# Kernel tuning notes

Measured on AMD Instinct MI355X. Metric: run time of the kernel, lower is better.

## Reference

```python
import jax, jax.numpy as jnp
import numpy as np

B, C, A, H, W = 8, 64, 32, 64, 64  # batch, input_nf, atten_nf, height, width

def setup_inputs() -> dict:
    key = jax.random.key(0)
    k = jax.random.split(key, 5)
    scale = 1.0 / np.sqrt(C)
    return {
        "x":  jax.random.normal(k[0], (B, C, H, W), dtype=jnp.float32),
        "Wg": jax.random.uniform(k[1], (A, C), jnp.float32, -scale, scale),  # 1x1 conv kernel
        "bg": jax.random.uniform(k[2], (A,),   jnp.float32, -scale, scale),
        "Wh": jax.random.uniform(k[3], (A, C), jnp.float32, -scale, scale),
        "bh": jax.random.uniform(k[4], (A,),   jnp.float32, -scale, scale),
    }

def reference(x, Wg, bg, Wh, bh):
    b, c, h, w = x.shape
    n = h * w
    xf = x.reshape(b, c, n)                               # [B, C, N]
    g = jnp.einsum('ac,bcn->ban', Wg, xf) + bg[None, :, None]  # 1x1 conv == GEMM
    hq = jnp.einsum('ac,bcn->ban', Wh, xf) + bh[None, :, None]
    scores = jnp.einsum('ban,bam->bnm', g, hq)            # [B, N, N]
    alpha = jax.nn.softmax(scores, axis=2)
    r = jnp.einsum('bnm,bcm->bcn', alpha, xf)             # alpha @ x^T, back to [B,C,N]
    r = r.reshape(b, c, h, w)
    r = r + x  # is_residual=True
    return (jax.nn.relu(r), alpha)
```

## Files before the change

kernel.cpp:

```cpp
#include <hip/hip_runtime.h>
#include <hip/hip_bf16.h>
#include <math.h>

#define NB 8
#define NC 64
#define NA 32
#define NN 4096
#define NWAVE 8

typedef __attribute__((ext_vector_type(8))) short bf16x8;
typedef __attribute__((ext_vector_type(4))) short bf16x4;
typedef __attribute__((ext_vector_type(4))) float f32x4;

#if __has_builtin(__builtin_amdgcn_mfma_f32_16x16x16bf16_1k)
  #define HAVE_MFMA16 1
  #define MFMA16(A,B,C) __builtin_amdgcn_mfma_f32_16x16x16bf16_1k(A,B,C,0,0,0)
#elif __has_builtin(__builtin_amdgcn_mfma_f32_16x16x16_bf16)
  #define HAVE_MFMA16 1
  #define MFMA16(A,B,C) __builtin_amdgcn_mfma_f32_16x16x16_bf16(A,B,C,0,0,0)
#else
  #define HAVE_MFMA16 0
#endif

__device__ inline ushort f2bf(float f) {
  union { float f; unsigned u; } v; v.f = f;
  unsigned r = v.u + 0x7fffu + ((v.u >> 16) & 1u);
  return (ushort)(r >> 16);
}

__device__ inline bf16x8 pack8(const f32x4 a, const f32x4 b) {
  union { ushort us[8]; bf16x8 v; } u;
#pragma unroll
  for (int i = 0; i < 4; ++i) { u.us[i] = f2bf(a[i]); u.us[4 + i] = f2bf(b[i]); }
  return u.v;
}

__device__ inline uint2 packbf(const f32x4 p) {
  uint2 q;
  q.x = (uint)f2bf(p[0]) | ((uint)f2bf(p[1]) << 16);
  q.y = (uint)f2bf(p[2]) | ((uint)f2bf(p[3]) << 16);
  return q;
}

#if HAVE_MFMA16
__device__ inline bf16x4 pk4(const f32x4 p) {
  union { uint u[2]; bf16x4 v; } t;
  asm("v_cvt_pk_bf16_f32 %0, %1, %2" : "=v"(t.u[0]) : "v"(p[0]), "v"(p[1]));
  asm("v_cvt_pk_bf16_f32 %0, %1, %2" : "=v"(t.u[1]) : "v"(p[2]), "v"(p[3]));
  return t.v;
}
#endif

__global__ __launch_bounds__(256) void prep_kernel(
    const float* __restrict__ x, const float* __restrict__ Wg, const float* __restrict__ bg,
    const float* __restrict__ Wh, const float* __restrict__ bh,
    ushort* __restrict__ gT, ushort* __restrict__ hqT, ushort* __restrict__ xfb2)
{
  __shared__ float wg_s[NA * NC];
  __shared__ float wh_s[NA * NC];
  const int t = threadIdx.x;
  for (int i = t; i < NA * NC; i += 256) { wg_s[i] = Wg[i]; wh_s[i] = Wh[i]; }
  __syncthreads();

  const int gid = blockIdx.x * 256 + t;
  const int b = gid >> 12;
  const int n = gid & (NN - 1);
  const float* xb = x + (size_t)b * NC * NN + n;
  const size_t x2base = (size_t)b * NC * NN + (size_t)(n >> 4) * (NC * 16) + (n & 15);

  float accg[NA], acch[NA];
#pragma unroll
  for (int a = 0; a < NA; ++a) { accg[a] = 0.f; acch[a] = 0.f; }

  for (int c4 = 0; c4 < NC / 4; ++c4) {
    const float xv0 = xb[(size_t)(c4 * 4 + 0) * NN];
    const float xv1 = xb[(size_t)(c4 * 4 + 1) * NN];
    const float xv2 = xb[(size_t)(c4 * 4 + 2) * NN];
    const float xv3 = xb[(size_t)(c4 * 4 + 3) * NN];
    xfb2[x2base + (size_t)(c4 * 4 + 0) * 16] = f2bf(xv0);
    xfb2[x2base + (size_t)(c4 * 4 + 1) * 16] = f2bf(xv1);
    xfb2[x2base + (size_t)(c4 * 4 + 2) * 16] = f2bf(xv2);
    xfb2[x2base + (size_t)(c4 * 4 + 3) * 16] = f2bf(xv3);
#pragma unroll
    for (int a = 0; a < NA; ++a) {
      const float4 wg4 = *(const float4*)&wg_s[a * NC + c4 * 4];
      const float4 wh4 = *(const float4*)&wh_s[a * NC + c4 * 4];
      accg[a] += wg4.x * xv0 + wg4.y * xv1 + wg4.z * xv2 + wg4.w * xv3;
      acch[a] += wh4.x * xv0 + wh4.y * xv1 + wh4.z * xv2 + wh4.w * xv3;
    }
  }

  const float LOG2E = 1.44269504088896340736f;
  ushort og[NA], oh[NA];
#pragma unroll
  for (int a = 0; a < NA; ++a) {
    og[a] = f2bf((accg[a] + bg[a]) * LOG2E);
    oh[a] = f2bf(acch[a] + bh[a]);
  }
  const size_t o = ((size_t)b * NN + n) * NA;
#pragma unroll
  for (int k = 0; k < 4; ++k) {
    uint4 vg, vh;
    vg.x = (uint)og[k*8+0] | ((uint)og[k*8+1] << 16);
    vg.y = (uint)og[k*8+2] | ((uint)og[k*8+3] << 16);
    vg.z = (uint)og[k*8+4] | ((uint)og[k*8+5] << 16);
    vg.w = (uint)og[k*8+6] | ((uint)og[k*8+7] << 16);
    vh.x = (uint)oh[k*8+0] | ((uint)oh[k*8+1] << 16);
    vh.y = (uint)oh[k*8+2] | ((uint)oh[k*8+3] << 16);
    vh.z = (uint)oh[k*8+4] | ((uint)oh[k*8+5] << 16);
    vh.w = (uint)oh[k*8+6] | ((uint)oh[k*8+7] << 16);
    *(uint4*)(gT  + o + k * 8) = vg;
    *(uint4*)(hqT + o + k * 8) = vh;
  }
}

__global__ __launch_bounds__(512, 4) void attn_kernel(
    const ushort* __restrict__ gT, const ushort* __restrict__ hqT,
    const ushort* __restrict__ xfb2, const float* __restrict__ x,
    float* __restrict__ outp, float* __restrict__ alpha)
{
  __shared__ float plds[NWAVE][32][32];
  __shared__ float rtile[32][65];
  __shared__ float Lp[NWAVE][32];
  __shared__ float LinvS[32];
#if !HAVE_MFMA16
  ushort (*pbuf)[32][36] = reinterpret_cast<ushort (*)[32][36]>(&plds[0][0][0]);
#endif

  const int tid = threadIdx.x;
  const int l  = tid & 63;
  const int w  = tid >> 6;
  const int lm = l & 15;
  const int lh = l >> 4;

  const int wgid = (blockIdx.x & 7) * 128 + (blockIdx.x >> 3);
  const int b  = wgid >> 7;
  const int n0 = (wgid & 127) << 5;

  const ushort* gB  = gT   + (size_t)b * NN * NA;
  const ushort* hB  = hqT  + (size_t)b * NN * NA;
  const ushort* xB2 = xfb2 + (size_t)b * NC * NN;

  bf16x8 gb0 = *(const bf16x8*)(gB + (size_t)(n0 + lm) * NA + lh * 8);
  bf16x8 gb1 = *(const bf16x8*)(gB + (size_t)(n0 + 16 + lm) * NA + lh * 8);
  const int mbase = w << 9;
  bf16x8 ha0 = *(const bf16x8*)(hB + (size_t)(mbase + lm) * NA + lh * 8);
  bf16x8 ha1 = *(const bf16x8*)(hB + (size_t)(mbase + 16 + lm) * NA + lh * 8);

  float* rflat = &rtile[0][0];
  for (int i = tid; i < 32 * 65; i += 512) rflat[i] = 0.f;

  const f32x4 zz = {0.f, 0.f, 0.f, 0.f};
  f32x4 racc[2][4];
#pragma unroll
  for (int gi = 0; gi < 2; ++gi)
#pragma unroll
    for (int ci = 0; ci < 4; ++ci) racc[gi][ci] = zz;

  float sume0 = 0.f, sume1 = 0.f;
  for (int mc = 0; mc < 16; ++mc) {
    const int m0 = mbase + (mc << 5);
    const int m1 = mbase + (((mc + 1) & 15) << 5);
    const int t0 = m0 >> 4;
    const bf16x8 na0 = *(const bf16x8*)(hB + (size_t)(m1 + lm) * NA + lh * 8);
    const bf16x8 na1 = *(const bf16x8*)(hB + (size_t)(m1 + 16 + lm) * NA + lh * 8);
#if HAVE_MFMA16
    bf16x4 xv0[4], xv1[4];
#pragma unroll
    for (int ci = 0; ci < 4; ++ci) {
      xv0[ci] = *(const bf16x4*)(xB2 + (size_t)t0       * (NC * 16) + (ci * 16 + lm) * 16 + lh * 4);
      xv1[ci] = *(const bf16x4*)(xB2 + (size_t)(t0 + 1) * (NC * 16) + (ci * 16 + lm) * 16 + lh * 4);
    }
#else
    bf16x8 xv[4];
#pragma unroll
    for (int ci = 0; ci < 4; ++ci)
      xv[ci] = *(const bf16x8*)(xB2 + (size_t)(t0 + (lh >> 1)) * (NC * 16) + (ci * 16 + lm) * 16 + (lh & 1) * 8);
#endif

    const f32x4 s00 = __builtin_amdgcn_mfma_f32_16x16x32_bf16(ha0, gb0, zz, 0, 0, 0);
    const f32x4 s10 = __builtin_amdgcn_mfma_f32_16x16x32_bf16(ha1, gb0, zz, 0, 0, 0);
    const f32x4 s01 = __builtin_amdgcn_mfma_f32_16x16x32_bf16(ha0, gb1, zz, 0, 0, 0);
    const f32x4 s11 = __builtin_amdgcn_mfma_f32_16x16x32_bf16(ha1, gb1, zz, 0, 0, 0);

    f32x4 e00, e10, e01, e11;
#pragma unroll
    for (int r = 0; r < 4; ++r) {
      e00[r] = exp2f(s00[r]);
      e10[r] = exp2f(s10[r]);
      e01[r] = exp2f(s01[r]);
      e11[r] = exp2f(s11[r]);
      sume0 += e00[r] + e10[r];
      sume1 += e01[r] + e11[r];
    }

#if HAVE_MFMA16
    const bf16x4 A00 = pk4(e00);
    const bf16x4 A01 = pk4(e10);
    const bf16x4 A10 = pk4(e01);
    const bf16x4 A11 = pk4(e11);
#pragma unroll
    for (int ci = 0; ci < 4; ++ci) {
      racc[0][ci] = MFMA16(A00, xv0[ci], racc[0][ci]);
      racc[0][ci] = MFMA16(A01, xv1[ci], racc[0][ci]);
      racc[1][ci] = MFMA16(A10, xv0[ci], racc[1][ci]);
      racc[1][ci] = MFMA16(A11, xv1[ci], racc[1][ci]);
    }
#else
    *(uint2*)&pbuf[w][lm][lh * 4]           = packbf(e00);
    *(uint2*)&pbuf[w][lm][16 + lh * 4]      = packbf(e10);
    *(uint2*)&pbuf[w][16 + lm][lh * 4]      = packbf(e01);
    *(uint2*)&pbuf[w][16 + lm][16 + lh * 4] = packbf(e11);
    union UB { uint4 u; bf16x8 v; } ua, ub;
    {
      const uint2 a0 = *(const uint2*)&pbuf[w][lm][lh * 8];
      const uint2 a1 = *(const uint2*)&pbuf[w][lm][lh * 8 + 4];
      ua.u = make_uint4(a0.x, a0.y, a1.x, a1.y);
      const uint2 b0 = *(const uint2*)&pbuf[w][16 + lm][lh * 8];
      const uint2 b1 = *(const uint2*)&pbuf[w][16 + lm][lh * 8 + 4];
      ub.u = make_uint4(b0.x, b0.y, b1.x, b1.y);
    }
#pragma unroll
    for (int ci = 0; ci < 4; ++ci) {
      racc[0][ci] = __builtin_amdgcn_mfma_f32_16x16x32_bf16(ua.v, xv[ci], racc[0][ci], 0, 0, 0);
      racc[1][ci] = __builtin_amdgcn_mfma_f32_16x16x32_bf16(ub.v, xv[ci], racc[1][ci], 0, 0, 0);
    }
#endif
    ha0 = na0; ha1 = na1;
  }

  sume0 += __shfl_xor(sume0, 16); sume0 += __shfl_xor(sume0, 32);
  sume1 += __shfl_xor(sume1, 16); sume1 += __shfl_xor(sume1, 32);
  if (l < 16) { Lp[w][l] = sume0; Lp[w][16 + l] = sume1; }
  __syncthreads();

  float Ls0 = 0.f, Ls1 = 0.f;
#pragma unroll
  for (int ww = 0; ww < NWAVE; ++ww) { Ls0 += Lp[ww][lm]; Ls1 += Lp[ww][16 + lm]; }
  const float blog0 = -log2f(Ls0);
  const float blog1 = -log2f(Ls1);

  if (tid < 32) {
    float s = 0.f;
#pragma unroll
    for (int ww = 0; ww < NWAVE; ++ww) s += Lp[ww][tid];
    LinvS[tid] = 1.0f / s;
  }

#pragma unroll
  for (int gi = 0; gi < 2; ++gi)
#pragma unroll
    for (int ci = 0; ci < 4; ++ci)
#pragma unroll
      for (int r = 0; r < 4; ++r)
        atomicAdd(&rtile[gi * 16 + lh * 4 + r][ci * 16 + lm], racc[gi][ci][r]);
  __syncthreads();

  {
    const int c  = tid >> 3;
    const int j4 = (tid & 7) << 2;
    f32x4 v;
#pragma unroll
    for (int k = 0; k < 4; ++k) v[k] = rtile[j4 + k][c] * LinvS[j4 + k];
    const size_t oo = ((size_t)b * NC + c) * NN + n0 + j4;
    const f32x4 xr = *(const f32x4*)(x + oo);
#pragma unroll
    for (int k = 0; k < 4; ++k) {
      const float t = v[k] + xr[k];
      v[k] = t > 0.f ? t : 0.f;
    }
    __builtin_nontemporal_store(v, (f32x4*)(outp + oo));
  }

  const f32x4 bias0 = {blog0, blog0, blog0, blog0};
  const f32x4 bias1 = {blog1, blog1, blog1, blog1};
  float* aB = alpha + ((size_t)b * NN + n0) * NN;
  const int k7   = lm & 7;
  const int nrow = l >> 3;
  const int uu   = l & 7;

  for (int mc = 0; mc < 16; ++mc) {
    const int m0 = mbase + (mc << 5);
    const int m1 = mbase + (((mc + 1) & 15) << 5);
    const bf16x8 na0 = *(const bf16x8*)(hB + (size_t)(m1 + lm) * NA + lh * 8);
    const bf16x8 na1 = *(const bf16x8*)(hB + (size_t)(m1 + 16 + lm) * NA + lh * 8);

    const f32x4 s00 = __builtin_amdgcn_mfma_f32_16x16x32_bf16(ha0, gb0, bias0, 0, 0, 0);
    const f32x4 s10 = __builtin_amdgcn_mfma_f32_16x16x32_bf16(ha1, gb0, bias0, 0, 0, 0);
    const f32x4 s01 = __builtin_amdgcn_mfma_f32_16x16x32_bf16(ha0, gb1, bias1, 0, 0, 0);
    const f32x4 s11 = __builtin_amdgcn_mfma_f32_16x16x32_bf16(ha1, gb1, bias1, 0, 0, 0);

    f32x4 p00, p10, p01, p11;
#pragma unroll
    for (int r = 0; r < 4; ++r) {
      p00[r] = exp2f(s00[r]);
      p10[r] = exp2f(s10[r]);
      p01[r] = exp2f(s01[r]);
      p11[r] = exp2f(s11[r]);
    }

    *(f32x4*)&plds[w][lm]     [((lh    ) ^ k7) << 2] = p00;
    *(f32x4*)&plds[w][lm]     [((lh + 4) ^ k7) << 2] = p10;
    *(f32x4*)&plds[w][16 + lm][((lh    ) ^ k7) << 2] = p01;
    *(f32x4*)&plds[w][16 + lm][((lh + 4) ^ k7) << 2] = p11;

#pragma unroll
    for (int j = 0; j < 4; ++j) {
      const int row = j * 8 + nrow;
      const f32x4 pv = *(const f32x4*)&plds[w][row][(uu ^ (row & 7)) << 2];
      __builtin_nontemporal_store(pv, (f32x4*)(aB + (size_t)row * NN + m0 + uu * 4));
    }
    ha0 = na0; ha1 = na1;
  }
}

extern "C" void kernel_launch(void* const* d_in, const int* in_sizes, int n_in,
                              void* d_out, int out_size, void* d_ws, size_t ws_size,
                              hipStream_t stream) {
  const float* x  = (const float*)d_in[0];
  const float* Wg = (const float*)d_in[1];
  const float* bg = (const float*)d_in[2];
  const float* Wh = (const float*)d_in[3];
  const float* bh = (const float*)d_in[4];

  float* outp  = (float*)d_out;
  float* alpha = outp + (size_t)NB * NC * NN;

  ushort* gT   = (ushort*)d_ws;
  ushort* hqT  = gT + (size_t)NB * NN * NA;
  ushort* xfb2 = hqT + (size_t)NB * NN * NA;

  prep_kernel<<<NB * NN / 256, 256, 0, stream>>>(x, Wg, bg, Wh, bh, gT, hqT, xfb2);
  attn_kernel<<<NB * (NN / 32), 512, 0, stream>>>(gT, hqT, xfb2, x, outp, alpha);
}
```

Before: 218.9 us.

## Split attention into row-sum/output kernel and separate alpha-writing kernel

Result: slower. 274.2 us (+25.2%).

```diff
diff --git a/kernel.cpp b/kernel.cpp
--- a/kernel.cpp
+++ b/kernel.cpp
@@ -114,17 +114,16 @@
   }
 }
 
-__global__ __launch_bounds__(512, 4) void attn_kernel(
+__global__ __launch_bounds__(512, 4) void rsum_kernel(
     const ushort* __restrict__ gT, const ushort* __restrict__ hqT,
     const ushort* __restrict__ xfb2, const float* __restrict__ x,
     float* __restrict__ outp, float* __restrict__ alpha)
 {
-  __shared__ float plds[NWAVE][32][32];
   __shared__ float rtile[32][65];
   __shared__ float Lp[NWAVE][32];
   __shared__ float LinvS[32];
 #if !HAVE_MFMA16
-  ushort (*pbuf)[32][36] = reinterpret_cast<ushort (*)[32][36]>(&plds[0][0][0]);
+  __shared__ ushort pbuf[NWAVE][32][36];
 #endif
 
   const int tid = threadIdx.x;
@@ -234,17 +233,12 @@
   if (l < 16) { Lp[w][l] = sume0; Lp[w][16 + l] = sume1; }
   __syncthreads();
 
-  float Ls0 = 0.f, Ls1 = 0.f;
-#pragma unroll
-  for (int ww = 0; ww < NWAVE; ++ww) { Ls0 += Lp[ww][lm]; Ls1 += Lp[ww][16 + lm]; }
-  const float blog0 = -log2f(Ls0);
-  const float blog1 = -log2f(Ls1);
-
   if (tid < 32) {
     float s = 0.f;
 #pragma unroll
     for (int ww = 0; ww < NWAVE; ++ww) s += Lp[ww][tid];
     LinvS[tid] = 1.0f / s;
+    alpha[((size_t)b * NN + n0 + tid) * NN] = -log2f(s);
   }
 
 #pragma unroll
@@ -256,25 +250,54 @@
         atomicAdd(&rtile[gi * 16 + lh * 4 + r][ci * 16 + lm], racc[gi][ci][r]);
   __syncthreads();
 
-  {
-    const int c  = tid >> 3;
-    const int j4 = (tid & 7) << 2;
-    f32x4 v;
-#pragma unroll
-    for (int k = 0; k < 4; ++k) v[k] = rtile[j4 + k][c] * LinvS[j4 + k];
-    const size_t oo = ((size_t)b * NC + c) * NN + n0 + j4;
-    const f32x4 xr = *(const f32x4*)(x + oo);
-#pragma unroll
-    for (int k = 0; k < 4; ++k) {
-      const float t = v[k] + xr[k];
-      v[k] = t > 0.f ? t : 0.f;
-    }
-    __builtin_nontemporal_store(v, (f32x4*)(outp + oo));
-  }
-
-  const f32x4 bias0 = {blog0, blog0, blog0, blog0};
-  const f32x4 bias1 = {blog1, blog1, blog1, blog1};
+  const int c  = tid >> 3;
+  const int j4 = (tid & 7) << 2;
+  f32x4 v;
+#pragma unroll
+  for (int k = 0; k < 4; ++k) v[k] = rtile[j4 + k][c] * LinvS[j4 + k];
+  const size_t oo = ((size_t)b * NC + c) * NN + n0 + j4;
+  const f32x4 xr = *(const f32x4*)(x + oo);
+#pragma unroll
+  for (int k = 0; k < 4; ++k) {
+    const float t = v[k] + xr[k];
+    v[k] = t > 0.f ? t : 0.f;
+  }
+  __builtin_nontemporal_store(v, (f32x4*)(outp + oo));
+}
+
+__global__ __launch_bounds__(512) void alpha_kernel(
+    const ushort* __restrict__ gT, const ushort* __restrict__ hqT,
+    float* __restrict__ alpha)
+{
+  __shared__ float plds[NWAVE][32][32];
+
+  const int tid = threadIdx.x;
+  const int l  = tid & 63;
+  const int w  = tid >> 6;
+  const int lm = l & 15;
+  const int lh = l >> 4;
+
+  const int wgid = (blockIdx.x & 7) * 128 + (blockIdx.x >> 3);
+  const int b  = wgid >> 7;
+  const int n0 = (wgid & 127) << 5;
+
+  const ushort* gB = gT  + (size_t)b * NN * NA;
+  const ushort* hB = hqT + (size_t)b * NN * NA;
   float* aB = alpha + ((size_t)b * NN + n0) * NN;
+
+  const float bl0 = aB[(size_t)lm * NN];
+  const float bl1 = aB[(size_t)(16 + lm) * NN];
+
+  bf16x8 gb0 = *(const bf16x8*)(gB + (size_t)(n0 + lm) * NA + lh * 8);
+  bf16x8 gb1 = *(const bf16x8*)(gB + (size_t)(n0 + 16 + lm) * NA + lh * 8);
+  const int mbase = w << 9;
+  bf16x8 ha0 = *(const bf16x8*)(hB + (size_t)(mbase + lm) * NA + lh * 8);
+  bf16x8 ha1 = *(const bf16x8*)(hB + (size_t)(mbase + 16 + lm) * NA + lh * 8);
+
+  __syncthreads();
+
+  const f32x4 bias0 = {bl0, bl0, bl0, bl0};
+  const f32x4 bias1 = {bl1, bl1, bl1, bl1};
   const int k7   = lm & 7;
   const int nrow = l >> 3;
   const int uu   = l & 7;
@@ -331,5 +354,6 @@
   ushort* xfb2 = hqT + (size_t)NB * NN * NA;
 
   prep_kernel<<<NB * NN / 256, 256, 0, stream>>>(x, Wg, bg, Wh, bh, gT, hqT, xfb2);
-  attn_kernel<<<NB * (NN / 32), 512, 0, stream>>>(gT, hqT, xfb2, x, outp, alpha);
-}
+  rsum_kernel<<<NB * (NN / 32), 512, 0, stream>>>(gT, hqT, xfb2, x, outp, alpha);
+  alpha_kernel<<<NB * (NN / 32), 512, 0, stream>>>(gT, hqT, alpha);
+}
```
